# Performance work log

Measured on AMD Instinct MI355X. Metric: run time of the kernel, lower is better.

The kernel has to match this reference:

```python
import jax, jax.numpy as jnp
import numpy as np

E = 300000
N_ATOMS = 10000
C = 256
RBF = 16
NUM_TARGET = 1


def setup_inputs() -> dict:
    key = jax.random.key(0)
    ks = jax.random.split(key, 12)
    s = lambda fan_in: 1.0 / np.sqrt(fan_in)
    return {
        "x": jax.random.normal(ks[0], (E, C), dtype=jnp.float32),
        "rbf": jax.random.uniform(ks[1], (E, RBF), dtype=jnp.float32),
        "num_atoms": N_ATOMS,
        "edge_index_0": jax.random.randint(ks[2], (E,), 0, N_ATOMS, dtype=jnp.int64),
        # lin_rbf: Linear(rbf_dim -> in_channels)
        "w_rbf": jax.random.normal(ks[3], (C, RBF), dtype=jnp.float32) * s(RBF),
        "b_rbf": jnp.zeros((C,), dtype=jnp.float32),
        # mlp: Linear(C,C), SiLU, Linear(C,C), SiLU, Linear(C, num_target)
        "w1": jax.random.normal(ks[4], (C, C), dtype=jnp.float32) * s(C),
        "b1": jnp.zeros((C,), dtype=jnp.float32),
        "w2": jax.random.normal(ks[5], (C, C), dtype=jnp.float32) * s(C),
        "b2": jnp.zeros((C,), dtype=jnp.float32),
        "w3": jax.random.normal(ks[6], (NUM_TARGET, C), dtype=jnp.float32) * s(C),
        "b3": jnp.zeros((NUM_TARGET,), dtype=jnp.float32),
    }


def reference(x, rbf, num_atoms, edge_index_0, w_rbf, b_rbf, w1, b1, w2, b2, w3, b3):
    # rbf_filter = lin_rbf(rbf): [E, C]
    rbf_filter = rbf @ w_rbf.T + b_rbf
    msg = rbf_filter * x  # [E, C]
    # scatter_add over edge source -> per-atom features [num_atoms, C]
    out = jax.ops.segment_sum(msg, edge_index_0, num_segments=num_atoms)
    # MLP: Linear+SiLU, Linear+SiLU, Linear
    out = jax.nn.silu(out @ w1.T + b1)
    out = jax.nn.silu(out @ w2.T + b2)
    out = out @ w3.T + b3  # [num_atoms, num_target]
    return out
```

## Files before the change

### kernel.cpp

```cpp
#include <hip/hip_runtime.h>
#include <math.h>

#define CDIM 256
#define RBFD 16
#define NATOMS 10000

__device__ __forceinline__ float dot4f(float4 a, float4 b) {
  return a.x * b.x + a.y * b.y + a.z * b.z + a.w * b.w;
}

__global__ void hist_kernel(const int* __restrict__ eidx, int* __restrict__ counts,
                            int E) {
  const int i = blockIdx.x * blockDim.x + threadIdx.x;
  if (i < E) atomicAdd(&counts[eidx[i]], 1);
}

__global__ void scan_kernel(const int* __restrict__ counts,
                            int* __restrict__ offsets, int* __restrict__ cursor) {
  __shared__ int part[256];
  const int t = threadIdx.x;
  const int CH = (NATOMS + 255) / 256;
  const int base = t * CH;
  const int n = min(CH, max(0, NATOMS - base));
  int s = 0;
  for (int j = 0; j < n; ++j) s += counts[base + j];
  part[t] = s;
  __syncthreads();
  for (int off = 1; off < 256; off <<= 1) {
    int v = 0;
    if (t >= off) v = part[t - off];
    __syncthreads();
    part[t] += v;
    __syncthreads();
  }
  int run = part[t] - s;
  for (int j = 0; j < n; ++j) {
    offsets[base + j] = run;
    cursor[base + j] = run;
    run += counts[base + j];
  }
  if (t == 255) offsets[NATOMS] = part[255];
}

__global__ void scatter_kernel(const int* __restrict__ eidx,
                               int* __restrict__ cursor, int* __restrict__ elist,
                               int E) {
  const int i = blockIdx.x * blockDim.x + threadIdx.x;
  if (i < E) {
    const int a = eidx[i];
    const int pos = atomicAdd(&cursor[a], 1);
    elist[pos] = i;
  }
}

__global__ __launch_bounds__(256, 4) void gather_kernel(
    const float* __restrict__ x, const float* __restrict__ rbf,
    const int* __restrict__ elist, const int* __restrict__ offsets,
    const float* __restrict__ w_rbf, const float* __restrict__ b_rbf,
    float* __restrict__ acc) {
  const int lane = threadIdx.x & 63;
  const int atom = (blockIdx.x * blockDim.x + threadIdx.x) >> 6;
  if (atom >= NATOMS) return;
  const int c0 = lane * 4;

  float4 wv[4][4];
  const float4 bb = *(const float4*)(b_rbf + c0);
#pragma unroll
  for (int j = 0; j < 4; ++j) {
    const float4* wr = (const float4*)(w_rbf + (size_t)(c0 + j) * RBFD);
    wv[j][0] = wr[0];
    wv[j][1] = wr[1];
    wv[j][2] = wr[2];
    wv[j][3] = wr[3];
  }

  const int start = offsets[atom];
  const int end = offsets[atom + 1];
  float4 sum = make_float4(0.f, 0.f, 0.f, 0.f);

  int e = (start < end) ? elist[start] : 0;
  for (int i = start; i < end; ++i) {
    const int e_next = (i + 1 < end) ? elist[i + 1] : 0;
    const float4* rp = (const float4*)(rbf + (size_t)e * RBFD);
    const float4 r0 = rp[0], r1 = rp[1], r2 = rp[2], r3 = rp[3];
    const float4 xx = *(const float4*)(x + (size_t)e * CDIM + c0);

    float4 f;
    f.x = bb.x + dot4f(wv[0][0], r0) + dot4f(wv[0][1], r1) +
          dot4f(wv[0][2], r2) + dot4f(wv[0][3], r3);
    f.y = bb.y + dot4f(wv[1][0], r0) + dot4f(wv[1][1], r1) +
          dot4f(wv[1][2], r2) + dot4f(wv[1][3], r3);
    f.z = bb.z + dot4f(wv[2][0], r0) + dot4f(wv[2][1], r1) +
          dot4f(wv[2][2], r2) + dot4f(wv[2][3], r3);
    f.w = bb.w + dot4f(wv[3][0], r0) + dot4f(wv[3][1], r1) +
          dot4f(wv[3][2], r2) + dot4f(wv[3][3], r3);

    sum.x += f.x * xx.x;
    sum.y += f.y * xx.y;
    sum.z += f.z * xx.z;
    sum.w += f.w * xx.w;
    e = e_next;
  }
  *(float4*)(acc + (size_t)atom * CDIM + c0) = sum;
}

__global__ void transpose_kernel(const float* __restrict__ w1,
                                 const float* __restrict__ w2,
                                 float* __restrict__ w1T,
                                 float* __restrict__ w2T) {
  __shared__ float tile[32][33];
  const float* src = blockIdx.z ? w2 : w1;
  float* dst = blockIdx.z ? w2T : w1T;
  const int bx = blockIdx.x * 32;
  const int by = blockIdx.y * 32;
  const int tx = threadIdx.x, ty = threadIdx.y;
#pragma unroll
  for (int i = 0; i < 32; i += 8)
    tile[ty + i][tx] = src[(size_t)(by + ty + i) * CDIM + bx + tx];
  __syncthreads();
#pragma unroll
  for (int i = 0; i < 32; i += 8)
    dst[(size_t)(bx + ty + i) * CDIM + by + tx] = tile[tx][ty + i];
}

__global__ __launch_bounds__(256, 2) void mlp_kernel(
    const float* __restrict__ hin, const float* __restrict__ w1T,
    const float* __restrict__ b1, const float* __restrict__ w2T,
    const float* __restrict__ b2, const float* __restrict__ w3,
    const float* __restrict__ b3, float* __restrict__ out, int natoms) {
  __shared__ float H[32 * 256];
  __shared__ float WK[32 * 256];
  const int tid = threadIdx.x;
  const int tc = tid & 31;
  const int ta = tid >> 5;
  const int a0 = blockIdx.x * 32;
  const int cA = tc * 4;
  const int cB = 128 + tc * 4;

  {
    const float4* src = (const float4*)hin + (size_t)a0 * 64;
    float4* Hv = (float4*)H;
#pragma unroll
    for (int i = 0; i < 8; ++i) {
      const int idx = tid + i * 256;
      const int ga = a0 + (idx >> 6);
      Hv[idx] = (ga < natoms) ? src[idx] : make_float4(0.f, 0.f, 0.f, 0.f);
    }
  }

  float s[4][8];

#pragma unroll 1
  for (int layer = 0; layer < 2; ++layer) {
    const float* wT = (layer == 0) ? w1T : w2T;
    const float* bias = (layer == 0) ? b1 : b2;
    float r[4][8];
    const float4 bA = *(const float4*)(bias + cA);
    const float4 bB = *(const float4*)(bias + cB);
#pragma unroll
    for (int a = 0; a < 4; ++a) {
      r[a][0] = bA.x; r[a][1] = bA.y; r[a][2] = bA.z; r[a][3] = bA.w;
      r[a][4] = bB.x; r[a][5] = bB.y; r[a][6] = bB.z; r[a][7] = bB.w;
    }

    for (int k0 = 0; k0 < 256; k0 += 32) {
      __syncthreads();
      {
        const float4* wsrc = (const float4*)(wT + (size_t)k0 * CDIM);
        float4* WKv = (float4*)WK;
#pragma unroll
        for (int i = 0; i < 8; ++i) WKv[tid + i * 256] = wsrc[tid + i * 256];
      }
      __syncthreads();

#pragma unroll
      for (int kk = 0; kk < 32; kk += 4) {
        float4 ha[4];
#pragma unroll
        for (int a = 0; a < 4; ++a)
          ha[a] = *(const float4*)&H[(ta * 4 + a) * 256 + k0 + kk];
#pragma unroll
        for (int u = 0; u < 4; ++u) {
          const float4 w0 = *(const float4*)&WK[(kk + u) * 256 + cA];
          const float4 w1v = *(const float4*)&WK[(kk + u) * 256 + cB];
#pragma unroll
          for (int a = 0; a < 4; ++a) {
            const float hv = (u == 0) ? ha[a].x
                           : (u == 1) ? ha[a].y
                           : (u == 2) ? ha[a].z : ha[a].w;
            r[a][0] += hv * w0.x;  r[a][1] += hv * w0.y;
            r[a][2] += hv * w0.z;  r[a][3] += hv * w0.w;
            r[a][4] += hv * w1v.x; r[a][5] += hv * w1v.y;
            r[a][6] += hv * w1v.z; r[a][7] += hv * w1v.w;
          }
        }
      }
    }

#pragma unroll
    for (int a = 0; a < 4; ++a)
#pragma unroll
      for (int j = 0; j < 8; ++j) {
        const float v = r[a][j];
        s[a][j] = v / (1.0f + __expf(-v));
      }

    if (layer == 0) {
      __syncthreads();
#pragma unroll
      for (int a = 0; a < 4; ++a) {
        *(float4*)&H[(ta * 4 + a) * 256 + cA] =
            make_float4(s[a][0], s[a][1], s[a][2], s[a][3]);
        *(float4*)&H[(ta * 4 + a) * 256 + cB] =
            make_float4(s[a][4], s[a][5], s[a][6], s[a][7]);
      }
    }
  }

  const float4 w3a = *(const float4*)(w3 + cA);
  const float4 w3b = *(const float4*)(w3 + cB);
  float part[4];
#pragma unroll
  for (int a = 0; a < 4; ++a) {
    part[a] = s[a][0] * w3a.x + s[a][1] * w3a.y + s[a][2] * w3a.z +
              s[a][3] * w3a.w + s[a][4] * w3b.x + s[a][5] * w3b.y +
              s[a][6] * w3b.z + s[a][7] * w3b.w;
  }
  __syncthreads();
  float* red = WK;
#pragma unroll
  for (int a = 0; a < 4; ++a) red[(ta * 4 + a) * 33 + tc] = part[a];
  __syncthreads();
  if (tid < 32) {
    float sum = 0.f;
#pragma unroll
    for (int j = 0; j < 32; ++j) sum += red[tid * 33 + j];
    const int ga = a0 + tid;
    if (ga < natoms) out[ga] = sum + b3[0];
  }
}

extern "C" void kernel_launch(void* const* d_in, const int* in_sizes, int n_in,
                              void* d_out, int out_size, void* d_ws,
                              size_t ws_size, hipStream_t stream) {
  const float* x = (const float*)d_in[0];
  const float* rbf = (const float*)d_in[1];
  const int* eidx = (const int*)d_in[3];
  const float* w_rbf = (const float*)d_in[4];
  const float* b_rbf = (const float*)d_in[5];
  const float* w1 = (const float*)d_in[6];
  const float* b1 = (const float*)d_in[7];
  const float* w2 = (const float*)d_in[8];
  const float* b2 = (const float*)d_in[9];
  const float* w3 = (const float*)d_in[10];
  const float* b3 = (const float*)d_in[11];
  float* out = (float*)d_out;
  const int E = in_sizes[0] / CDIM;

  char* p = (char*)d_ws;
  float* acc = (float*)p;              p += (size_t)NATOMS * CDIM * sizeof(float);
  float* w1T = (float*)p;              p += CDIM * CDIM * sizeof(float);
  float* w2T = (float*)p;              p += CDIM * CDIM * sizeof(float);
  int* counts = (int*)p;               p += NATOMS * sizeof(int);
  int* offsets = (int*)p;              p += (NATOMS + 1) * sizeof(int);
  int* cursor = (int*)p;               p += NATOMS * sizeof(int);
  int* elist = (int*)p;                p += (size_t)E * sizeof(int);

  hipMemsetAsync(counts, 0, NATOMS * sizeof(int), stream);
  hist_kernel<<<(E + 255) / 256, 256, 0, stream>>>(eidx, counts, E);
  scan_kernel<<<1, 256, 0, stream>>>(counts, offsets, cursor);
  scatter_kernel<<<(E + 255) / 256, 256, 0, stream>>>(eidx, cursor, elist, E);
  transpose_kernel<<<dim3(8, 8, 2), dim3(32, 8), 0, stream>>>(w1, w2, w1T, w2T);
  gather_kernel<<<(NATOMS * 64 + 255) / 256, 256, 0, stream>>>(
      x, rbf, elist, offsets, w_rbf, b_rbf, acc);
  mlp_kernel<<<(NATOMS + 31) / 32, 256, 0, stream>>>(acc, w1T, b1, w2T, b2, w3,
                                                     b3, out, NATOMS);
}
```

Baseline: 663.4 us.

## Pipeline gather loads through an LDS ring via direct global-to-LDS loads

The per-atom gather loop now streams each edge's x row and rbf vector into a per-wave 8-deep LDS ring using global_load_lds, with hand-written waitcnt and ds_read_b128 in inline asm. This keeps many global loads in flight per wave to hide gather latency, where before only one edge index was prefetched at a time. Edge indices are made wave-uniform with readfirstlane, and two accumulators split the dependency chain. The cost is 40KB of LDS per block, which caps occupancy, plus fragile manual vmcnt bookkeeping that depends on the compiler issuing no other vector memory ops inside the loop.

```diff
diff --git a/kernel.cpp b/kernel.cpp
--- a/kernel.cpp
+++ b/kernel.cpp
@@ -5,7 +5,9 @@
 #define RBFD 16
 #define NATOMS 10000
 
-__device__ __forceinline__ float dot4f(float4 a, float4 b) {
+typedef float f32x4 __attribute__((ext_vector_type(4)));
+
+__device__ __forceinline__ float dot4e(float4 a, f32x4 b) {
   return a.x * b.x + a.y * b.y + a.z * b.z + a.w * b.w;
 }
 
@@ -53,15 +55,24 @@
   }
 }
 
-__global__ __launch_bounds__(256, 4) void gather_kernel(
+#define SLOT_BYTES 1280
+#define RING_DEPTH 8
+
+__global__ __launch_bounds__(256) void gather_kernel(
     const float* __restrict__ x, const float* __restrict__ rbf,
     const int* __restrict__ elist, const int* __restrict__ offsets,
     const float* __restrict__ w_rbf, const float* __restrict__ b_rbf,
     float* __restrict__ acc) {
-  const int lane = threadIdx.x & 63;
-  const int atom = (blockIdx.x * blockDim.x + threadIdx.x) >> 6;
+  __shared__ __align__(16) char ring[4 * RING_DEPTH * SLOT_BYTES];
+  const int tid = threadIdx.x;
+  const int lane = tid & 63;
+  const int atom = (blockIdx.x * blockDim.x + tid) >> 6;
   if (atom >= NATOMS) return;
+  const int wbase = (tid >> 6) * (RING_DEPTH * SLOT_BYTES);
   const int c0 = lane * 4;
+
+  const int start = __builtin_amdgcn_readfirstlane(offsets[atom]);
+  const int end = __builtin_amdgcn_readfirstlane(offsets[atom + 1]);
 
   float4 wv[4][4];
   const float4 bb = *(const float4*)(b_rbf + c0);
@@ -74,33 +85,146 @@
     wv[j][3] = wr[3];
   }
 
-  const int start = offsets[atom];
-  const int end = offsets[atom + 1];
-  float4 sum = make_float4(0.f, 0.f, 0.f, 0.f);
-
-  int e = (start < end) ? elist[start] : 0;
-  for (int i = start; i < end; ++i) {
-    const int e_next = (i + 1 < end) ? elist[i + 1] : 0;
-    const float4* rp = (const float4*)(rbf + (size_t)e * RBFD);
-    const float4 r0 = rp[0], r1 = rp[1], r2 = rp[2], r3 = rp[3];
-    const float4 xx = *(const float4*)(x + (size_t)e * CDIM + c0);
-
-    float4 f;
-    f.x = bb.x + dot4f(wv[0][0], r0) + dot4f(wv[0][1], r1) +
-          dot4f(wv[0][2], r2) + dot4f(wv[0][3], r3);
-    f.y = bb.y + dot4f(wv[1][0], r0) + dot4f(wv[1][1], r1) +
-          dot4f(wv[1][2], r2) + dot4f(wv[1][3], r3);
-    f.z = bb.z + dot4f(wv[2][0], r0) + dot4f(wv[2][1], r1) +
-          dot4f(wv[2][2], r2) + dot4f(wv[2][3], r3);
-    f.w = bb.w + dot4f(wv[3][0], r0) + dot4f(wv[3][1], r1) +
-          dot4f(wv[3][2], r2) + dot4f(wv[3][3], r3);
-
-    sum.x += f.x * xx.x;
-    sum.y += f.y * xx.y;
-    sum.z += f.z * xx.z;
-    sum.w += f.w * xx.w;
-    e = e_next;
-  }
+  if (end <= start) {
+    *(float4*)(acc + (size_t)atom * CDIM + c0) = make_float4(0.f, 0.f, 0.f, 0.f);
+    return;
+  }
+  const int last = end - 1;
+
+  const unsigned ring_off =
+      (unsigned)(size_t)(__attribute__((address_space(3))) char*)ring;
+  const unsigned vax = ring_off + wbase + lane * 16;
+  const unsigned vau = ring_off + wbase + 1024;
+
+#define PREFETCH(J, eid)                                                      \
+  {                                                                           \
+    const int e_ = __builtin_amdgcn_readfirstlane(eid);                       \
+    __builtin_amdgcn_global_load_lds(                                         \
+        (const __attribute__((address_space(1))) void*)(x + (size_t)e_ * CDIM \
+                                                        + lane * 4),          \
+        (__attribute__((address_space(3))) void*)(ring + wbase +              \
+                                                  (J)*SLOT_BYTES),            \
+        16, 0, 0);                                                            \
+    __builtin_amdgcn_global_load_lds(                                         \
+        (const __attribute__((address_space(1))) void*)(                      \
+            rbf + (size_t)e_ * RBFD + (lane & 15)),                           \
+        (__attribute__((address_space(3))) void*)(ring + wbase +              \
+                                                  (J)*SLOT_BYTES + 1024),     \
+        4, 0, 0);                                                             \
+  }
+
+#define COMPUTE_BODY(sum)                                                     \
+  {                                                                           \
+    float4 f_;                                                                \
+    f_.x = bb.x + dot4e(wv[0][0], r0) + dot4e(wv[0][1], r1) +                 \
+           dot4e(wv[0][2], r2) + dot4e(wv[0][3], r3);                         \
+    f_.y = bb.y + dot4e(wv[1][0], r0) + dot4e(wv[1][1], r1) +                 \
+           dot4e(wv[1][2], r2) + dot4e(wv[1][3], r3);                         \
+    f_.z = bb.z + dot4e(wv[2][0], r0) + dot4e(wv[2][1], r1) +                 \
+           dot4e(wv[2][2], r2) + dot4e(wv[2][3], r3);                         \
+    f_.w = bb.w + dot4e(wv[3][0], r0) + dot4e(wv[3][1], r1) +                 \
+           dot4e(wv[3][2], r2) + dot4e(wv[3][3], r3);                         \
+    sum.x += f_.x * xv.x;                                                     \
+    sum.y += f_.y * xv.y;                                                     \
+    sum.z += f_.z * xv.z;                                                     \
+    sum.w += f_.w * xv.w;                                                     \
+  }
+
+#define CONSUME(J, sum)                                                       \
+  {                                                                           \
+    f32x4 xv, r0, r1, r2, r3;                                                 \
+    const unsigned ax_ = vax + (J)*SLOT_BYTES;                                \
+    const unsigned au_ = vau + (J)*SLOT_BYTES;                                \
+    asm volatile(                                                             \
+        "s_waitcnt vmcnt(12)\n\t"                                             \
+        "ds_read_b128 %0, %5\n\t"                                             \
+        "ds_read_b128 %1, %6\n\t"                                             \
+        "ds_read_b128 %2, %6 offset:16\n\t"                                   \
+        "ds_read_b128 %3, %6 offset:32\n\t"                                   \
+        "ds_read_b128 %4, %6 offset:48\n\t"                                   \
+        "s_waitcnt lgkmcnt(0)"                                                \
+        : "=&v"(xv), "=&v"(r0), "=&v"(r1), "=&v"(r2), "=&v"(r3)               \
+        : "v"(ax_), "v"(au_)                                                  \
+        : "memory");                                                          \
+    __builtin_amdgcn_sched_barrier(0);                                        \
+    COMPUTE_BODY(sum)                                                         \
+  }
+
+#define CONSUME_NW(J, sum)                                                    \
+  {                                                                           \
+    f32x4 xv, r0, r1, r2, r3;                                                 \
+    const unsigned ax_ = vax + (J)*SLOT_BYTES;                                \
+    const unsigned au_ = vau + (J)*SLOT_BYTES;                                \
+    asm volatile(                                                             \
+        "ds_read_b128 %0, %5\n\t"                                             \
+        "ds_read_b128 %1, %6\n\t"                                             \
+        "ds_read_b128 %2, %6 offset:16\n\t"                                   \
+        "ds_read_b128 %3, %6 offset:32\n\t"                                   \
+        "ds_read_b128 %4, %6 offset:48\n\t"                                   \
+        "s_waitcnt lgkmcnt(0)"                                                \
+        : "=&v"(xv), "=&v"(r0), "=&v"(r1), "=&v"(r2), "=&v"(r3)               \
+        : "v"(ax_), "v"(au_)                                                  \
+        : "memory");                                                          \
+    __builtin_amdgcn_sched_barrier(0);                                        \
+    COMPUTE_BODY(sum)                                                         \
+  }
+
+  float4 sumA = make_float4(0.f, 0.f, 0.f, 0.f);
+  float4 sumB = make_float4(0.f, 0.f, 0.f, 0.f);
+
+  int id0[RING_DEPTH];
+#pragma unroll
+  for (int j = 0; j < RING_DEPTH; ++j)
+    id0[j] = __builtin_amdgcn_readfirstlane(elist[min(start + j, last)]);
+
+  int idr[RING_DEPTH];
+#pragma unroll
+  for (int j = 0; j < RING_DEPTH; ++j) {
+    PREFETCH(j, id0[j])
+    __builtin_amdgcn_sched_barrier(0);
+    idr[j] = __builtin_amdgcn_readfirstlane(
+        elist[min(start + RING_DEPTH + j, last)]);
+  }
+
+  int i = start;
+  for (; i + RING_DEPTH <= end; i += RING_DEPTH) {
+#pragma unroll
+    for (int j = 0; j < RING_DEPTH; ++j) {
+      if (j & 1) {
+        CONSUME(j, sumB)
+      } else {
+        CONSUME(j, sumA)
+      }
+      PREFETCH(j, idr[j])
+      __builtin_amdgcn_sched_barrier(0);
+      idr[j] = __builtin_amdgcn_readfirstlane(
+          elist[min(i + 2 * RING_DEPTH + j, last)]);
+    }
+  }
+
+  asm volatile("s_waitcnt vmcnt(0)" ::: "memory");
+  const int rem = end - i;
+#pragma unroll
+  for (int j = 0; j < RING_DEPTH; ++j) {
+    if (j < rem) {
+      if (j & 1) {
+        CONSUME_NW(j, sumB)
+      } else {
+        CONSUME_NW(j, sumA)
+      }
+    }
+  }
+
+#undef PREFETCH
+#undef COMPUTE_BODY
+#undef CONSUME
+#undef CONSUME_NW
+
+  float4 sum;
+  sum.x = sumA.x + sumB.x;
+  sum.y = sumA.y + sumB.y;
+  sum.z = sumA.z + sumB.z;
+  sum.w = sumA.w + sumB.w;
   *(float4*)(acc + (size_t)atom * CDIM + c0) = sum;
 }
 
```

Measured after the change: 638.9 us. 3.7% less time.

## Replace CSR sort-and-gather with edge-parallel atomic scatter into accumulator

Applied to the files above, without the earlier changes.

Drops the histogram, scan and scatter kernels that built a per-atom edge list. Each wavefront now streams edges in order, computing the rbf filter and atomically adding filter*x into the per-atom accumulator. Edge loads are double-buffered across iterations. This removes three launches and the random gather of x rows in exchange for 256 float atomics per edge into a 10 MB accumulator that must be zeroed first, and it makes summation order nondeterministic.

```diff
diff --git a/kernel.cpp b/kernel.cpp
--- a/kernel.cpp
+++ b/kernel.cpp
@@ -5,103 +5,102 @@
 #define RBFD 16
 #define NATOMS 10000
 
-__device__ __forceinline__ float dot4f(float4 a, float4 b) {
+__device__ __forceinline__ float dot44(float4 a, float4 b) {
   return a.x * b.x + a.y * b.y + a.z * b.z + a.w * b.w;
 }
 
-__global__ void hist_kernel(const int* __restrict__ eidx, int* __restrict__ counts,
-                            int E) {
-  const int i = blockIdx.x * blockDim.x + threadIdx.x;
-  if (i < E) atomicAdd(&counts[eidx[i]], 1);
-}
-
-__global__ void scan_kernel(const int* __restrict__ counts,
-                            int* __restrict__ offsets, int* __restrict__ cursor) {
-  __shared__ int part[256];
-  const int t = threadIdx.x;
-  const int CH = (NATOMS + 255) / 256;
-  const int base = t * CH;
-  const int n = min(CH, max(0, NATOMS - base));
-  int s = 0;
-  for (int j = 0; j < n; ++j) s += counts[base + j];
-  part[t] = s;
-  __syncthreads();
-  for (int off = 1; off < 256; off <<= 1) {
-    int v = 0;
-    if (t >= off) v = part[t - off];
-    __syncthreads();
-    part[t] += v;
-    __syncthreads();
-  }
-  int run = part[t] - s;
-  for (int j = 0; j < n; ++j) {
-    offsets[base + j] = run;
-    cursor[base + j] = run;
-    run += counts[base + j];
-  }
-  if (t == 255) offsets[NATOMS] = part[255];
-}
-
-__global__ void scatter_kernel(const int* __restrict__ eidx,
-                               int* __restrict__ cursor, int* __restrict__ elist,
-                               int E) {
-  const int i = blockIdx.x * blockDim.x + threadIdx.x;
-  if (i < E) {
-    const int a = eidx[i];
-    const int pos = atomicAdd(&cursor[a], 1);
-    elist[pos] = i;
-  }
-}
-
-__global__ __launch_bounds__(256, 4) void gather_kernel(
+__global__ __launch_bounds__(256, 3) void edge_gather_kernel(
     const float* __restrict__ x, const float* __restrict__ rbf,
-    const int* __restrict__ elist, const int* __restrict__ offsets,
-    const float* __restrict__ w_rbf, const float* __restrict__ b_rbf,
-    float* __restrict__ acc) {
-  const int lane = threadIdx.x & 63;
-  const int atom = (blockIdx.x * blockDim.x + threadIdx.x) >> 6;
-  if (atom >= NATOMS) return;
-  const int c0 = lane * 4;
-
-  float4 wv[4][4];
-  const float4 bb = *(const float4*)(b_rbf + c0);
-#pragma unroll
-  for (int j = 0; j < 4; ++j) {
-    const float4* wr = (const float4*)(w_rbf + (size_t)(c0 + j) * RBFD);
-    wv[j][0] = wr[0];
-    wv[j][1] = wr[1];
-    wv[j][2] = wr[2];
-    wv[j][3] = wr[3];
-  }
-
-  const int start = offsets[atom];
-  const int end = offsets[atom + 1];
-  float4 sum = make_float4(0.f, 0.f, 0.f, 0.f);
-
-  int e = (start < end) ? elist[start] : 0;
-  for (int i = start; i < end; ++i) {
-    const int e_next = (i + 1 < end) ? elist[i + 1] : 0;
-    const float4* rp = (const float4*)(rbf + (size_t)e * RBFD);
-    const float4 r0 = rp[0], r1 = rp[1], r2 = rp[2], r3 = rp[3];
-    const float4 xx = *(const float4*)(x + (size_t)e * CDIM + c0);
-
-    float4 f;
-    f.x = bb.x + dot4f(wv[0][0], r0) + dot4f(wv[0][1], r1) +
-          dot4f(wv[0][2], r2) + dot4f(wv[0][3], r3);
-    f.y = bb.y + dot4f(wv[1][0], r0) + dot4f(wv[1][1], r1) +
-          dot4f(wv[1][2], r2) + dot4f(wv[1][3], r3);
-    f.z = bb.z + dot4f(wv[2][0], r0) + dot4f(wv[2][1], r1) +
-          dot4f(wv[2][2], r2) + dot4f(wv[2][3], r3);
-    f.w = bb.w + dot4f(wv[3][0], r0) + dot4f(wv[3][1], r1) +
-          dot4f(wv[3][2], r2) + dot4f(wv[3][3], r3);
-
-    sum.x += f.x * xx.x;
-    sum.y += f.y * xx.y;
-    sum.z += f.z * xx.z;
-    sum.w += f.w * xx.w;
-    e = e_next;
-  }
-  *(float4*)(acc + (size_t)atom * CDIM + c0) = sum;
+    const int* __restrict__ eidx, const float* __restrict__ w_rbf,
+    const float* __restrict__ b_rbf, float* __restrict__ acc, int E) {
+  const int tid = threadIdx.x;
+  const int lane = tid & 63;
+  const int wid = __builtin_amdgcn_readfirstlane(
+      (int)((blockIdx.x * blockDim.x + tid) >> 6));
+  const int nw = (int)((gridDim.x * blockDim.x) >> 6);
+
+  float4 w0q0, w0q1, w0q2, w0q3;
+  float4 w1q0, w1q1, w1q2, w1q3;
+  float4 w2q0, w2q1, w2q2, w2q3;
+  float4 w3q0, w3q1, w3q2, w3q3;
+  {
+    const float4* r;
+    r = (const float4*)(w_rbf + (size_t)(lane)*RBFD);
+    w0q0 = r[0]; w0q1 = r[1]; w0q2 = r[2]; w0q3 = r[3];
+    r = (const float4*)(w_rbf + (size_t)(64 + lane) * RBFD);
+    w1q0 = r[0]; w1q1 = r[1]; w1q2 = r[2]; w1q3 = r[3];
+    r = (const float4*)(w_rbf + (size_t)(128 + lane) * RBFD);
+    w2q0 = r[0]; w2q1 = r[1]; w2q2 = r[2]; w2q3 = r[3];
+    r = (const float4*)(w_rbf + (size_t)(192 + lane) * RBFD);
+    w3q0 = r[0]; w3q1 = r[1]; w3q2 = r[2]; w3q3 = r[3];
+  }
+  const float b0 = b_rbf[lane];
+  const float b1 = b_rbf[64 + lane];
+  const float b2 = b_rbf[128 + lane];
+  const float b3 = b_rbf[192 + lane];
+
+  int aA, aB;
+  float xA0, xA1, xA2, xA3, xB0, xB1, xB2, xB3;
+  float4 rA0, rA1, rA2, rA3, rB0, rB1, rB2, rB3;
+
+#define LOADE(S, e)                                                          \
+  {                                                                          \
+    a##S = __builtin_amdgcn_readfirstlane(eidx[e]);                          \
+    const float* xp_ = x + (size_t)(e)*CDIM + lane;                          \
+    x##S##0 = xp_[0];                                                        \
+    x##S##1 = xp_[64];                                                       \
+    x##S##2 = xp_[128];                                                      \
+    x##S##3 = xp_[192];                                                      \
+    const float4* q_ = (const float4*)(rbf + (size_t)(e)*RBFD);              \
+    r##S##0 = q_[0];                                                         \
+    r##S##1 = q_[1];                                                         \
+    r##S##2 = q_[2];                                                         \
+    r##S##3 = q_[3];                                                         \
+  }
+
+#define FIRE(S)                                                              \
+  {                                                                          \
+    const float f0_ = b0 + dot44(w0q0, r##S##0) + dot44(w0q1, r##S##1) +     \
+                      dot44(w0q2, r##S##2) + dot44(w0q3, r##S##3);           \
+    const float f1_ = b1 + dot44(w1q0, r##S##0) + dot44(w1q1, r##S##1) +     \
+                      dot44(w1q2, r##S##2) + dot44(w1q3, r##S##3);           \
+    const float f2_ = b2 + dot44(w2q0, r##S##0) + dot44(w2q1, r##S##1) +     \
+                      dot44(w2q2, r##S##2) + dot44(w2q3, r##S##3);           \
+    const float f3_ = b3 + dot44(w3q0, r##S##0) + dot44(w3q1, r##S##1) +     \
+                      dot44(w3q2, r##S##2) + dot44(w3q3, r##S##3);           \
+    float* d_ = acc + (size_t)a##S * CDIM + lane;                            \
+    atomicAdd(d_ + 0, f0_ * x##S##0);                                        \
+    atomicAdd(d_ + 64, f1_ * x##S##1);                                       \
+    atomicAdd(d_ + 128, f2_ * x##S##2);                                      \
+    atomicAdd(d_ + 192, f3_ * x##S##3);                                      \
+  }
+
+  int e = wid;
+  if (e >= E) return;
+  LOADE(A, e)
+  while (true) {
+    const int en = e + nw;
+    if (en < E) {
+      LOADE(B, en)
+      FIRE(A)
+      const int en2 = en + nw;
+      if (en2 < E) {
+        LOADE(A, en2)
+        FIRE(B)
+        e = en2;
+        continue;
+      } else {
+        FIRE(B)
+        break;
+      }
+    } else {
+      FIRE(A)
+      break;
+    }
+  }
+
+#undef LOADE
+#undef FIRE
 }
 
 __global__ void transpose_kernel(const float* __restrict__ w1,
@@ -261,18 +260,11 @@
   float* acc = (float*)p;              p += (size_t)NATOMS * CDIM * sizeof(float);
   float* w1T = (float*)p;              p += CDIM * CDIM * sizeof(float);
   float* w2T = (float*)p;              p += CDIM * CDIM * sizeof(float);
-  int* counts = (int*)p;               p += NATOMS * sizeof(int);
-  int* offsets = (int*)p;              p += (NATOMS + 1) * sizeof(int);
-  int* cursor = (int*)p;               p += NATOMS * sizeof(int);
-  int* elist = (int*)p;                p += (size_t)E * sizeof(int);
-
-  hipMemsetAsync(counts, 0, NATOMS * sizeof(int), stream);
-  hist_kernel<<<(E + 255) / 256, 256, 0, stream>>>(eidx, counts, E);
-  scan_kernel<<<1, 256, 0, stream>>>(counts, offsets, cursor);
-  scatter_kernel<<<(E + 255) / 256, 256, 0, stream>>>(eidx, cursor, elist, E);
+
+  (void)hipMemsetAsync(acc, 0, (size_t)NATOMS * CDIM * sizeof(float), stream);
   transpose_kernel<<<dim3(8, 8, 2), dim3(32, 8), 0, stream>>>(w1, w2, w1T, w2T);
-  gather_kernel<<<(NATOMS * 64 + 255) / 256, 256, 0, stream>>>(
-      x, rbf, elist, offsets, w_rbf, b_rbf, acc);
+  edge_gather_kernel<<<1024, 256, 0, stream>>>(x, rbf, eidx, w_rbf, b_rbf, acc,
+                                               E);
   mlp_kernel<<<(NATOMS + 31) / 32, 256, 0, stream>>>(acc, w1T, b1, w2T, b2, w3,
                                                      b3, out, NATOMS);
 }
```

After: 671.4 us. No clear change (+1.2%).
